# Kernel tuning notes

Measured on AMD Instinct MI355X. Metric: run time of the kernel, lower is better.

## Reference

```python
import jax, jax.numpy as jnp
import numpy as np


def setup_inputs() -> dict:
    key = jax.random.key(0)
    kq, kk, kv = jax.random.split(key, 3)
    N, L, H, D = 2, 2048, 16, 64
    Q = jax.random.normal(kq, (N, L, H, D), dtype=jnp.float32)
    K = jax.random.normal(kk, (N, L, H, D), dtype=jnp.float32)
    V = jax.random.normal(kv, (N, L, H, D), dtype=jnp.float32)
    return {"Q": Q, "K": K, "V": V}


def reference(Q, K, V):
    # Q: [N, l_q, H, d], K: [N, l_k, H, d], V: [N, l_k, H, d_v]
    d_key = K.shape[-1]
    scale = 1.0 / jnp.sqrt(jnp.asarray(d_key, dtype=Q.dtype))
    # scores: [N, l_q, l_k, H] (matches torch sum over d, softmax over l_k)
    scores = jnp.einsum("nqhd,nkhd->nqkh", Q, K) * scale
    attn = jax.nn.softmax(scores, axis=2)
    # out: [N, l_q, H, d_v]
    out = jnp.einsum("nqkh,nkhd->nqhd", attn, V)
    return out
```

## Files before the change

kernel.cpp:

```cpp
#include <hip/hip_runtime.h>
#include <hip/hip_bf16.h>

typedef __attribute__((ext_vector_type(8))) short bf16x8;
typedef __attribute__((ext_vector_type(4))) float float4_t;
typedef __attribute__((ext_vector_type(2))) float f32x2;
typedef __attribute__((ext_vector_type(16))) float f32x16;
typedef __attribute__((ext_vector_type(4))) int int4v;
typedef __attribute__((ext_vector_type(2))) int int2v;

constexpr int Lseq = 2048;
constexpr int ROWS = 1024;
constexpr float SCALE_LOG2E = 0.18033688011112042f;

__device__ short g_Kb[32 * 32 * 4096];
__device__ short g_Vb[32 * 32 * 4096];

__device__ __forceinline__ int cvtpk(float lo, float hi) {
  int r; asm("v_cvt_pk_bf16_f32 %0, %1, %2" : "=v"(r) : "v"(lo), "v"(hi)); return r;
}
__device__ __forceinline__ f32x2 pkadd(f32x2 a, f32x2 b) {
  f32x2 r; asm("v_pk_add_f32 %0, %1, %2" : "=v"(r) : "v"(a), "v"(b)); return r;
}
__device__ __forceinline__ void plswap(int& a, int& b) {
  int2v r = __builtin_amdgcn_permlane32_swap(a, b, false, false);
  a = r[0]; b = r[1];
}
__device__ __forceinline__ int4v pk8(float4_t a, float4_t b) {
  int4v t;
  t[0] = cvtpk(a[0], a[1]); t[1] = cvtpk(a[2], a[3]);
  t[2] = cvtpk(b[0], b[1]); t[3] = cvtpk(b[2], b[3]);
  return t;
}
__device__ __forceinline__ void dma16(const void* g, void* l) {
  __builtin_amdgcn_global_load_lds(
      (const __attribute__((address_space(1))) void*)g,
      (__attribute__((address_space(3))) void*)l, 16, 0, 0);
}

#define MFMA32(A, B, C) __builtin_amdgcn_mfma_f32_32x32x16_bf16((A), (B), (C), 0, 0, 0)

__global__ __launch_bounds__(256)
void preconv(const float* __restrict__ Kg, const float* __restrict__ Vg) {
  const int bid = blockIdx.x;
  const int nh = bid >> 5;
  const int kt = bid & 31;
  const size_t base = (size_t)(nh >> 4) * Lseq * ROWS + (size_t)(nh & 15) * 64;
  const int tid = threadIdx.x;
  char* kimg = (char*)g_Kb + ((size_t)nh * 32 + kt) * 8192;
  char* vimg = (char*)g_Vb + ((size_t)nh * 32 + kt) * 8192;

  {
    const int row = tid >> 2;
    const float* src = Kg + base + (size_t)(kt * 64 + row) * ROWS + (tid & 3) * 16;
    float4_t a = ((const float4_t*)src)[0];
    float4_t b = ((const float4_t*)src)[1];
    float4_t c = ((const float4_t*)src)[2];
    float4_t d = ((const float4_t*)src)[3];
    const int swz = (row & 7) << 4;
    const int wb  = row * 128 + (tid & 3) * 32;
    *(int4v*)(kimg + (wb ^ swz))        = pk8(a, b);
    *(int4v*)(kimg + ((wb + 16) ^ swz)) = pk8(c, d);
  }
  {
    const int d0 = tid & 63;
    const int lb = tid >> 6;
    const float* src = Vg + base + (size_t)(kt * 64 + lb * 16) * ROWS + d0;
    float v[16];
#pragma unroll
    for (int j = 0; j < 16; ++j) v[j] = src[(size_t)j * ROWS];
    int4v w0, w1;
    w0[0] = cvtpk(v[0], v[1]);   w0[1] = cvtpk(v[2], v[3]);
    w0[2] = cvtpk(v[4], v[5]);   w0[3] = cvtpk(v[6], v[7]);
    w1[0] = cvtpk(v[8], v[9]);   w1[1] = cvtpk(v[10], v[11]);
    w1[2] = cvtpk(v[12], v[13]); w1[3] = cvtpk(v[14], v[15]);
    const int swz = (d0 & 7) << 4;
    const int wb  = d0 * 128 + lb * 32;
    *(int4v*)(vimg + (wb ^ swz))        = w0;
    *(int4v*)(vimg + ((wb + 16) ^ swz)) = w1;
  }
}

__global__ __launch_bounds__(128, 2)
void attn_fwd(const float* __restrict__ Qg, float* __restrict__ Og) {
  __shared__ __align__(16) short kv_lds[2][2][64 * 64];

  const int wg  = blockIdx.x;
  const int swz = (wg & 7) * 128 + (wg >> 3);
  const int nh  = swz >> 5;
  const int qt  = swz & 31;
  const size_t base = (size_t)(nh >> 4) * Lseq * ROWS + (size_t)(nh & 15) * 64;

  const int tid  = threadIdx.x;
  const int lane = tid & 63;
  const int wid  = tid >> 6;
  const int lq   = lane & 31;
  const int hi   = lane >> 5;

  const char* gsrc = (const char*)(wid == 0 ? g_Kb : g_Vb) + (size_t)nh * (32 * 8192)
                     + lane * 16;
  auto stage = [&](int buf, int t) {
    const char* s = gsrc + (size_t)t * 8192;
    char* d = (char*)&kv_lds[buf][wid][0];
#pragma unroll
    for (int i = 0; i < 8; ++i) dma16(s + i * 1024, d + i * 1024);
  };

  stage(0, 0);

  bf16x8 qf[4];
  {
    const float* qrow = Qg + base + (size_t)(qt * 64 + wid * 32 + lq) * ROWS + hi * 8;
#pragma unroll
    for (int c = 0; c < 4; ++c) {
      float4_t a = *(const float4_t*)(qrow + c * 16);
      float4_t b = *(const float4_t*)(qrow + c * 16 + 4);
#pragma unroll
      for (int j = 0; j < 4; ++j) { a[j] *= SCALE_LOG2E; b[j] *= SCALE_LOG2E; }
      qf[c] = __builtin_bit_cast(bf16x8, pk8(a, b));
    }
  }

  const int rsw = (lq & 7) << 4;
  const int rb0 = lq * 128 + hi * 16;
  const int rb1 = (32 + lq) * 128 + hi * 16;

  float l = 0.f;
  f32x16 acc0, acc1;
#pragma unroll
  for (int r = 0; r < 16; ++r) { acc0[r] = 0.f; acc1[r] = 0.f; }

  asm volatile("s_waitcnt vmcnt(0)" ::: "memory");
  __syncthreads();

  int cur = 0;
  for (int t = 0; t < 32; ++t) {
    if (t < 31) stage(cur ^ 1, t + 1);

    f32x16 s0 = {}, s1 = {};
    const char* kld = (const char*)&kv_lds[cur][0][0];
    __builtin_amdgcn_s_setprio(1);
#pragma unroll
    for (int c = 0; c < 4; ++c) {
      bf16x8 ka = *(const bf16x8*)(kld + ((rb0 + c * 32) ^ rsw));
      s0 = MFMA32(ka, qf[c], s0);
    }
#pragma unroll
    for (int c = 0; c < 4; ++c) {
      bf16x8 ka = *(const bf16x8*)(kld + ((rb1 + c * 32) ^ rsw));
      s1 = MFMA32(ka, qf[c], s1);
    }
    __builtin_amdgcn_s_setprio(0);

#pragma unroll
    for (int r = 0; r < 16; ++r) {
      s0[r] = __builtin_amdgcn_exp2f(s0[r]);
      s1[r] = __builtin_amdgcn_exp2f(s1[r]);
    }

    bf16x8 pa[4];
#pragma unroll
    for (int c = 0; c < 4; ++c) {
      const f32x16& sv = (c < 2) ? s0 : s1;
      const int br = (c & 1) * 8;
      int t0 = cvtpk(sv[br + 0], sv[br + 1]);
      int t1 = cvtpk(sv[br + 2], sv[br + 3]);
      int t2 = cvtpk(sv[br + 4], sv[br + 5]);
      int t3 = cvtpk(sv[br + 6], sv[br + 7]);
      plswap(t0, t2);
      plswap(t1, t3);
      int4v tt; tt[0] = t0; tt[1] = t1; tt[2] = t2; tt[3] = t3;
      pa[c] = __builtin_bit_cast(bf16x8, tt);
    }

#define S2(v, i) (f32x2{(v)[2 * (i)], (v)[2 * (i) + 1]})
    {
      f32x2 u0 = pkadd(S2(s0, 0), S2(s0, 1));
      f32x2 u1 = pkadd(S2(s0, 2), S2(s0, 3));
      f32x2 u2 = pkadd(S2(s0, 4), S2(s0, 5));
      f32x2 u3 = pkadd(S2(s0, 6), S2(s0, 7));
      f32x2 u4 = pkadd(S2(s1, 0), S2(s1, 1));
      f32x2 u5 = pkadd(S2(s1, 2), S2(s1, 3));
      f32x2 u6 = pkadd(S2(s1, 4), S2(s1, 5));
      f32x2 u7 = pkadd(S2(s1, 6), S2(s1, 7));
      u0 = pkadd(u0, u1); u2 = pkadd(u2, u3);
      u4 = pkadd(u4, u5); u6 = pkadd(u6, u7);
      u0 = pkadd(u0, u2); u4 = pkadd(u4, u6);
      u0 = pkadd(u0, u4);
      l += u0[0] + u0[1];
    }
#undef S2

    const char* vld = (const char*)&kv_lds[cur][1][0];
    __builtin_amdgcn_s_setprio(1);
#pragma unroll
    for (int c = 0; c < 4; ++c) {
      bf16x8 vb = *(const bf16x8*)(vld + ((rb0 + c * 32) ^ rsw));
      acc0 = MFMA32(pa[c], vb, acc0);
    }
#pragma unroll
    for (int c = 0; c < 4; ++c) {
      bf16x8 vb = *(const bf16x8*)(vld + ((rb1 + c * 32) ^ rsw));
      acc1 = MFMA32(pa[c], vb, acc1);
    }
    __builtin_amdgcn_s_setprio(0);

    asm volatile("s_waitcnt vmcnt(0)" ::: "memory");
    __syncthreads();
    cur ^= 1;
  }

  {
    int a = __float_as_int(l), b = a;
    plswap(a, b);
    l = __int_as_float(a) + __int_as_float(b);
  }
  float linv = 1.0f / l;
#pragma unroll
  for (int r = 0; r < 16; ++r) {
    int qr = (r & 3) + 8 * (r >> 2) + 4 * hi;
    float li = __shfl(linv, qr);
    float* orow = Og + base + (size_t)(qt * 64 + wid * 32 + qr) * ROWS;
    orow[lq]      = acc0[r] * li;
    orow[32 + lq] = acc1[r] * li;
  }
}

extern "C" void kernel_launch(void* const* d_in, const int* in_sizes, int n_in,
                              void* d_out, int out_size, void* d_ws, size_t ws_size,
                              hipStream_t stream) {
  const float* Q = (const float*)d_in[0];
  const float* K = (const float*)d_in[1];
  const float* V = (const float*)d_in[2];
  float* O = (float*)d_out;
  preconv<<<dim3(1024), dim3(256), 0, stream>>>(K, V);
  attn_fwd<<<dim3(1024), dim3(128), 0, stream>>>(Q, O);
}
```

Baseline: 64.58 us.

## Load pre-laid-out K/V fragments straight to registers with buffer loads, drop LDS

The preconversion kernel now writes K and V bf16 images in the exact per-lane MFMA fragment order. The attention kernel then loads them straight into registers with raw buffer_load_dwordx4, double-buffering through vmcnt waits, instead of DMA to LDS plus barriers. Workgroups shrink to one wavefront per 32 query rows, doubling the grid to 2048. This removes LDS traffic and __syncthreads, but each wave now fetches all K/V itself with no sharing. That doubles global/L2 reads and raises register pressure.

```diff
diff --git a/kernel.cpp b/kernel.cpp
--- a/kernel.cpp
+++ b/kernel.cpp
@@ -7,6 +7,7 @@
 typedef __attribute__((ext_vector_type(16))) float f32x16;
 typedef __attribute__((ext_vector_type(4))) int int4v;
 typedef __attribute__((ext_vector_type(2))) int int2v;
+typedef __attribute__((ext_vector_type(4))) unsigned uint4v;
 
 constexpr int Lseq = 2048;
 constexpr int ROWS = 1024;
@@ -31,10 +32,30 @@
   t[2] = cvtpk(b[0], b[1]); t[3] = cvtpk(b[2], b[3]);
   return t;
 }
-__device__ __forceinline__ void dma16(const void* g, void* l) {
-  __builtin_amdgcn_global_load_lds(
-      (const __attribute__((address_space(1))) void*)g,
-      (__attribute__((address_space(3))) void*)l, 16, 0, 0);
+__device__ __forceinline__ uint4v make_srsrc(const void* p) {
+  unsigned long long a = (unsigned long long)p;
+  uint4v r; r[0] = (unsigned)a; r[1] = (unsigned)(a >> 32) & 0xffffu;
+  r[2] = 0xffffffffu; r[3] = 0x00020000u;
+  return r;
+}
+__device__ __forceinline__ void load8(int4v* dst, unsigned vo, uint4v rs) {
+  unsigned vo2 = vo + 4096u;
+  asm volatile(
+      "buffer_load_dwordx4 %0, %8, %9, 0 offen\n\t"
+      "buffer_load_dwordx4 %1, %8, %9, 0 offen offset:1024\n\t"
+      "buffer_load_dwordx4 %2, %8, %9, 0 offen offset:2048\n\t"
+      "buffer_load_dwordx4 %3, %8, %9, 0 offen offset:3072\n\t"
+      "buffer_load_dwordx4 %4, %10, %9, 0 offen\n\t"
+      "buffer_load_dwordx4 %5, %10, %9, 0 offen offset:1024\n\t"
+      "buffer_load_dwordx4 %6, %10, %9, 0 offen offset:2048\n\t"
+      "buffer_load_dwordx4 %7, %10, %9, 0 offen offset:3072"
+      : "=v"(dst[0]), "=v"(dst[1]), "=v"(dst[2]), "=v"(dst[3]),
+        "=v"(dst[4]), "=v"(dst[5]), "=v"(dst[6]), "=v"(dst[7])
+      : "v"(vo), "s"(rs), "v"(vo2));
+}
+__device__ __forceinline__ void wait8() {
+  asm volatile("s_waitcnt vmcnt(8)" ::: "memory");
+  __builtin_amdgcn_sched_barrier(0);
 }
 
 #define MFMA32(A, B, C) __builtin_amdgcn_mfma_f32_32x32x16_bf16((A), (B), (C), 0, 0, 0)
@@ -49,67 +70,49 @@
   char* kimg = (char*)g_Kb + ((size_t)nh * 32 + kt) * 8192;
   char* vimg = (char*)g_Vb + ((size_t)nh * 32 + kt) * 8192;
 
-  {
-    const int row = tid >> 2;
-    const float* src = Kg + base + (size_t)(kt * 64 + row) * ROWS + (tid & 3) * 16;
-    float4_t a = ((const float4_t*)src)[0];
-    float4_t b = ((const float4_t*)src)[1];
-    float4_t c = ((const float4_t*)src)[2];
-    float4_t d = ((const float4_t*)src)[3];
-    const int swz = (row & 7) << 4;
-    const int wb  = row * 128 + (tid & 3) * 32;
-    *(int4v*)(kimg + (wb ^ swz))        = pk8(a, b);
-    *(int4v*)(kimg + ((wb + 16) ^ swz)) = pk8(c, d);
-  }
-  {
-    const int d0 = tid & 63;
-    const int lb = tid >> 6;
-    const float* src = Vg + base + (size_t)(kt * 64 + lb * 16) * ROWS + d0;
-    float v[16];
-#pragma unroll
-    for (int j = 0; j < 16; ++j) v[j] = src[(size_t)j * ROWS];
-    int4v w0, w1;
-    w0[0] = cvtpk(v[0], v[1]);   w0[1] = cvtpk(v[2], v[3]);
-    w0[2] = cvtpk(v[4], v[5]);   w0[3] = cvtpk(v[6], v[7]);
-    w1[0] = cvtpk(v[8], v[9]);   w1[1] = cvtpk(v[10], v[11]);
-    w1[2] = cvtpk(v[12], v[13]); w1[3] = cvtpk(v[14], v[15]);
-    const int swz = (d0 & 7) << 4;
-    const int wb  = d0 * 128 + lb * 32;
-    *(int4v*)(vimg + (wb ^ swz))        = w0;
-    *(int4v*)(vimg + ((wb + 16) ^ swz)) = w1;
-  }
-}
-
-__global__ __launch_bounds__(128, 2)
+#pragma unroll
+  for (int p = 0; p < 2; ++p) {
+    const int f    = tid + p * 256;
+    const int half = f >> 8;
+    const int c    = (f >> 6) & 3;
+    const int hi   = (f >> 5) & 1;
+    const int lq   = f & 31;
+    {
+      const float* src = Kg + base + (size_t)(kt * 64 + half * 32 + lq) * ROWS
+                         + c * 16 + hi * 8;
+      float4_t a = *(const float4_t*)src;
+      float4_t b = *(const float4_t*)(src + 4);
+      *(int4v*)(kimg + f * 16) = pk8(a, b);
+    }
+    {
+      const float* src = Vg + base + (size_t)(kt * 64 + c * 16 + hi * 8) * ROWS
+                         + half * 32 + lq;
+      float v[8];
+#pragma unroll
+      for (int j = 0; j < 8; ++j) v[j] = src[(size_t)j * ROWS];
+      int4v w;
+      w[0] = cvtpk(v[0], v[1]); w[1] = cvtpk(v[2], v[3]);
+      w[2] = cvtpk(v[4], v[5]); w[3] = cvtpk(v[6], v[7]);
+      *(int4v*)(vimg + f * 16) = w;
+    }
+  }
+}
+
+__global__ __launch_bounds__(64, 2)
 void attn_fwd(const float* __restrict__ Qg, float* __restrict__ Og) {
-  __shared__ __align__(16) short kv_lds[2][2][64 * 64];
-
   const int wg  = blockIdx.x;
-  const int swz = (wg & 7) * 128 + (wg >> 3);
-  const int nh  = swz >> 5;
-  const int qt  = swz & 31;
+  const int swz = (wg & 7) * 256 + (wg >> 3);
+  const int nh  = swz >> 6;
+  const int qt  = swz & 63;
   const size_t base = (size_t)(nh >> 4) * Lseq * ROWS + (size_t)(nh & 15) * 64;
 
-  const int tid  = threadIdx.x;
-  const int lane = tid & 63;
-  const int wid  = tid >> 6;
+  const int lane = threadIdx.x;
   const int lq   = lane & 31;
   const int hi   = lane >> 5;
 
-  const char* gsrc = (const char*)(wid == 0 ? g_Kb : g_Vb) + (size_t)nh * (32 * 8192)
-                     + lane * 16;
-  auto stage = [&](int buf, int t) {
-    const char* s = gsrc + (size_t)t * 8192;
-    char* d = (char*)&kv_lds[buf][wid][0];
-#pragma unroll
-    for (int i = 0; i < 8; ++i) dma16(s + i * 1024, d + i * 1024);
-  };
-
-  stage(0, 0);
-
   bf16x8 qf[4];
   {
-    const float* qrow = Qg + base + (size_t)(qt * 64 + wid * 32 + lq) * ROWS + hi * 8;
+    const float* qrow = Qg + base + (size_t)(qt * 32 + lq) * ROWS + hi * 8;
 #pragma unroll
     for (int c = 0; c < 4; ++c) {
       float4_t a = *(const float4_t*)(qrow + c * 16);
@@ -119,37 +122,37 @@
       qf[c] = __builtin_bit_cast(bf16x8, pk8(a, b));
     }
   }
-
-  const int rsw = (lq & 7) << 4;
-  const int rb0 = lq * 128 + hi * 16;
-  const int rb1 = (32 + lq) * 128 + hi * 16;
+  asm volatile("s_waitcnt vmcnt(0)" ::: "memory");
+  __builtin_amdgcn_sched_barrier(0);
+
+  const uint4v rsK = make_srsrc((const char*)g_Kb + (size_t)nh * 262144);
+  const uint4v rsV = make_srsrc((const char*)g_Vb + (size_t)nh * 262144);
+  const unsigned voA = (unsigned)(lane * 16);
+
+  int4v kf[8], vf[8];
+  load8(kf, voA, rsK);
+  load8(vf, voA, rsV);
 
   float l = 0.f;
-  f32x16 acc0, acc1;
-#pragma unroll
-  for (int r = 0; r < 16; ++r) { acc0[r] = 0.f; acc1[r] = 0.f; }
-
-  asm volatile("s_waitcnt vmcnt(0)" ::: "memory");
-  __syncthreads();
-
-  int cur = 0;
+  f32x16 acc0 = {}, acc1 = {};
+  unsigned vo = voA;
+
+#pragma unroll 1
   for (int t = 0; t < 32; ++t) {
-    if (t < 31) stage(cur ^ 1, t + 1);
+    const unsigned vnext = (t < 31) ? vo + 8192u : voA;
+
+    wait8();
 
     f32x16 s0 = {}, s1 = {};
-    const char* kld = (const char*)&kv_lds[cur][0][0];
     __builtin_amdgcn_s_setprio(1);
 #pragma unroll
     for (int c = 0; c < 4; ++c) {
-      bf16x8 ka = *(const bf16x8*)(kld + ((rb0 + c * 32) ^ rsw));
-      s0 = MFMA32(ka, qf[c], s0);
-    }
-#pragma unroll
-    for (int c = 0; c < 4; ++c) {
-      bf16x8 ka = *(const bf16x8*)(kld + ((rb1 + c * 32) ^ rsw));
-      s1 = MFMA32(ka, qf[c], s1);
+      s0 = MFMA32(__builtin_bit_cast(bf16x8, kf[c]),     qf[c], s0);
+      s1 = MFMA32(__builtin_bit_cast(bf16x8, kf[4 + c]), qf[c], s1);
     }
     __builtin_amdgcn_s_setprio(0);
+
+    load8(kf, vnext, rsK);
 
 #pragma unroll
     for (int r = 0; r < 16; ++r) {
@@ -190,24 +193,22 @@
     }
 #undef S2
 
-    const char* vld = (const char*)&kv_lds[cur][1][0];
+    wait8();
+
     __builtin_amdgcn_s_setprio(1);
 #pragma unroll
     for (int c = 0; c < 4; ++c) {
-      bf16x8 vb = *(const bf16x8*)(vld + ((rb0 + c * 32) ^ rsw));
-      acc0 = MFMA32(pa[c], vb, acc0);
-    }
-#pragma unroll
-    for (int c = 0; c < 4; ++c) {
-      bf16x8 vb = *(const bf16x8*)(vld + ((rb1 + c * 32) ^ rsw));
-      acc1 = MFMA32(pa[c], vb, acc1);
+      acc0 = MFMA32(pa[c], __builtin_bit_cast(bf16x8, vf[c]),     acc0);
+      acc1 = MFMA32(pa[c], __builtin_bit_cast(bf16x8, vf[4 + c]), acc1);
     }
     __builtin_amdgcn_s_setprio(0);
 
-    asm volatile("s_waitcnt vmcnt(0)" ::: "memory");
-    __syncthreads();
-    cur ^= 1;
-  }
+    load8(vf, vnext, rsV);
+    vo = vnext;
+  }
+
+  asm volatile("s_waitcnt vmcnt(0)" ::: "memory");
+  __builtin_amdgcn_sched_barrier(0);
 
   {
     int a = __float_as_int(l), b = a;
@@ -219,7 +220,7 @@
   for (int r = 0; r < 16; ++r) {
     int qr = (r & 3) + 8 * (r >> 2) + 4 * hi;
     float li = __shfl(linv, qr);
-    float* orow = Og + base + (size_t)(qt * 64 + wid * 32 + qr) * ROWS;
+    float* orow = Og + base + (size_t)(qt * 32 + qr) * ROWS;
     orow[lq]      = acc0[r] * li;
     orow[32 + lq] = acc1[r] * li;
   }
@@ -233,5 +234,5 @@
   const float* V = (const float*)d_in[2];
   float* O = (float*)d_out;
   preconv<<<dim3(1024), dim3(256), 0, stream>>>(K, V);
-  attn_fwd<<<dim3(1024), dim3(128), 0, stream>>>(Q, O);
-}
+  attn_fwd<<<dim3(2048), dim3(64), 0, stream>>>(Q, O);
+}
```

After: 61.95 us. 1.04x faster.
